# Kernel tuning notes

Hardware: AMD Instinct MI355X
Metric: run time of the kernel (lower is better)

Reference implementation:

```python
import jax, jax.numpy as jnp
import numpy as np

B, BUFF, STK, NCOMP, HIST = 128, 64, 48, 8, 96
VOCAB, WDIM, POSN, POSD = 100000, 300, 50, 50
DEP, CAD, HAD, FC, U = 40, 50, 50, 128, 256
NOUT = 2 + 2 * DEP


def setup_inputs() -> dict:
    key = jax.random.key(0)
    ks = jax.random.split(key, 40)
    d = {}
    d['buff_word_id'] = jax.random.randint(ks[0], (B, BUFF), 0, VOCAB)
    d['buff_pos_id'] = jax.random.randint(ks[1], (B, BUFF), 0, POSN)
    d['comp_word_id'] = jax.random.randint(ks[2], (B, STK, 2 * NCOMP), 0, VOCAB)
    d['comp_pos_id'] = jax.random.randint(ks[3], (B, STK, 2 * NCOMP), 0, POSN)
    d['comp_action_id'] = jax.random.randint(ks[4], (B, STK, NCOMP), 0, 2 * DEP)
    d['comp_action_len'] = jax.random.randint(ks[5], (B, STK), 0, NCOMP + 1)
    d['history_action_id'] = jax.random.randint(ks[6], (B, HIST), 0, 3 + 4 * DEP)
    d['stack_length'] = jax.random.randint(ks[7], (B,), 1, STK + 1)
    d['buff_length'] = jax.random.randint(ks[8], (B,), 1, BUFF + 1)
    d['history_action_length'] = jax.random.randint(ks[9], (B,), 1, HIST + 1)

    def w(k, shape):
        return jax.random.normal(k, shape, jnp.float32) / np.sqrt(shape[0])

    d['p_emb'] = jax.random.normal(ks[10], (POSN, POSD), jnp.float32) * 0.1
    d['comp_a_emb'] = jax.random.normal(ks[11], (2 * DEP, CAD), jnp.float32) * 0.1
    d['hist_a_emb'] = jax.random.normal(ks[12], (3 + 4 * DEP, HAD), jnp.float32) * 0.1
    d['w_emb'] = jax.random.normal(ks[13], (VOCAB, WDIM), jnp.float32) * 0.1
    d['emb_W'] = w(ks[14], (WDIM + POSD, FC)); d['emb_b'] = jnp.zeros((FC,), jnp.float32)
    d['rec_W'] = w(ks[15], (FC + CAD + FC, FC)); d['rec_b'] = jnp.zeros((FC,), jnp.float32)
    d['sW0'] = w(ks[16], (FC + U, 4 * U)); d['sb0'] = jnp.zeros((4 * U,), jnp.float32)
    d['sW1'] = w(ks[17], (U + U, 4 * U)); d['sb1'] = jnp.zeros((4 * U,), jnp.float32)
    d['bW0'] = w(ks[18], (FC + U, 4 * U)); d['bb0'] = jnp.zeros((4 * U,), jnp.float32)
    d['bW1'] = w(ks[19], (U + U, 4 * U)); d['bb1'] = jnp.zeros((4 * U,), jnp.float32)
    d['aW0'] = w(ks[20], (HAD + U, 4 * U)); d['ab0'] = jnp.zeros((4 * U,), jnp.float32)
    d['aW1'] = w(ks[21], (U + U, 4 * U)); d['ab1'] = jnp.zeros((4 * U,), jnp.float32)
    d['fW'] = w(ks[22], (3 * U, NOUT)); d['fb'] = jnp.zeros((NOUT,), jnp.float32)
    return d


def _lstm_cell(c, h, x, W, b):
    # TF LSTMCell gate order: i, j (candidate), f, o; forget_bias = 1.0
    z = jnp.concatenate([x, h], -1) @ W + b
    i, j, f, o = jnp.split(z, 4, -1)
    c = c * jax.nn.sigmoid(f + 1.0) + jax.nn.sigmoid(i) * jnp.tanh(j)
    h = jnp.tanh(c) * jax.nn.sigmoid(o)
    return c, h


def _run_lstm2(x, lengths, W0, b0, W1, b1):
    # x: [B, T, D]; returns final (at t = length) second-layer h, like dynamic_rnn's state[1].h
    Bb, T, _ = x.shape
    u = W0.shape[1] // 4
    init = tuple(jnp.zeros((Bb, u), x.dtype) for _ in range(4))

    def step(carry, inp):
        xt, t = inp
        c0, h0, c1, h1 = carry
        nc0, nh0 = _lstm_cell(c0, h0, xt, W0, b0)
        nc1, nh1 = _lstm_cell(c1, h1, nh0, W1, b1)
        m = (t < lengths)[:, None]
        new = tuple(jnp.where(m, n, o) for n, o in zip((nc0, nh0, nc1, nh1), carry))
        return new, None

    (c0, h0, c1, h1), _ = jax.lax.scan(step, init, (x.transpose(1, 0, 2), jnp.arange(T)))
    return h1


def _compose(word_id, comp_emb, act_emb, a_len, rec_W, rec_b):
    # word_id: [2N] int, comp_emb: [2N, FC], act_emb: [N, CAD], a_len: scalar
    # Sequential dict-keyed recursive composition (dict keys are head word ids).
    N = act_emb.shape[0]
    head_ids = word_id[0::2]
    dep_ids = word_id[1::2]
    idxs = jnp.arange(N)

    def step(vals, n):
        mask_h = (head_ids == head_ids[n]) & (idxs < n)
        mask_d = (head_ids == dep_ids[n]) & (idxs < n)
        ih = jnp.max(jnp.where(mask_h, idxs, -1))
        idd = jnp.max(jnp.where(mask_d, idxs, -1))
        head_e = jnp.where(ih >= 0, vals[jnp.maximum(ih, 0)], comp_emb[2 * n])
        dep_e = jnp.where(idd >= 0, vals[jnp.maximum(idd, 0)], comp_emb[2 * n + 1])
        new = jnp.tanh(jnp.concatenate([head_e, act_emb[n], dep_e]) @ rec_W + rec_b)
        return vals.at[n].set(new), new

    vals0 = jnp.zeros((N, rec_W.shape[1]), comp_emb.dtype)
    _, news = jax.lax.scan(step, vals0, idxs)
    return jnp.where(a_len == 0, comp_emb[0], news[jnp.maximum(a_len - 1, 0)])


def reference(buff_word_id, buff_pos_id, comp_word_id, comp_pos_id, comp_action_id,
              comp_action_len, history_action_id, stack_length, buff_length,
              history_action_length, p_emb, comp_a_emb, hist_a_emb, w_emb,
              emb_W, emb_b, rec_W, rec_b, sW0, sb0, sW1, sb1, bW0, bb0, bW1, bb1,
              aW0, ab0, aW1, ab1, fW, fb):
    buff_emb = jax.nn.relu(
        jnp.concatenate([w_emb[buff_word_id], p_emb[buff_pos_id]], -1) @ emb_W + emb_b)
    comp_emb = jax.nn.relu(
        jnp.concatenate([w_emb[comp_word_id], p_emb[comp_pos_id]], -1) @ emb_W + emb_b)
    act_emb = comp_a_emb[comp_action_id]        # [B, STK, N, CAD]
    hist_emb = hist_a_emb[history_action_id]    # [B, HIST, HAD]

    comp_fn = lambda wi, ce, ae, al: _compose(wi, ce, ae, al, rec_W, rec_b)
    stack_emb = jax.vmap(jax.vmap(comp_fn))(comp_word_id, comp_emb, act_emb, comp_action_len)

    h_s = _run_lstm2(stack_emb, stack_length, sW0, sb0, sW1, sb1)
    h_b = _run_lstm2(buff_emb, buff_length, bW0, bb0, bW1, bb1)
    h_a = _run_lstm2(hist_emb, history_action_length, aW0, ab0, aW1, ab1)
    return jnp.concatenate([h_s, h_b, h_a], -1) @ fW + fb
```

## Files before the change

kernel.cpp:

```cpp
#include <hip/hip_runtime.h>

#define BB    128
#define BUFF  64
#define STK   48
#define NCOMP 8
#define HIST  96
#define WDIM  300
#define POSD  50
#define CAD   50
#define HAD   50
#define FC    128
#define UU    256
#define NOUT  82

typedef __bf16 bf16;
typedef __attribute__((ext_vector_type(8))) __bf16 bf16x8;
typedef __attribute__((ext_vector_type(4))) float   f32x4;

__device__ __forceinline__ float sigf(float x)   { return 1.f / (1.f + __expf(-x)); }
__device__ __forceinline__ float tanhf_(float x) { return 1.f - 2.f / (1.f + __expf(2.f * x)); }

__device__ __forceinline__ unsigned pack2(const float* p) {
  union { unsigned u; bf16 h[2]; } r;
  r.h[0] = (bf16)p[0]; r.h[1] = (bf16)p[1];
  return r.u;
}

__global__ __launch_bounds__(256) void k_emb(
    const int* bw, const int* bp, const int* cw, const int* cp,
    const float* w_emb, const float* p_emb, const float* embW, const float* embB,
    bf16* comp_emb, bf16* buff_emb)
{
  __shared__ __align__(16) char sm[138752];
  bf16*  A  = (bf16*)sm;
  bf16*  Wt = (bf16*)(sm + 46080);
  float* sb = (float*)(sm + 46080 + 92160);

  const int tid = threadIdx.x;
  const int r0  = blockIdx.x * 64;

  for (int i = tid; i < 64 * 176; i += 256) {
    int m = i / 176, c2 = i % 176, e0 = 2 * c2;
    int r = r0 + m;
    unsigned v;
    if (e0 < 300) {
      int word = (r < 98304) ? cw[r] : bw[r - 98304];
      v = pack2(w_emb + word * 300 + e0);
    } else if (e0 < 350) {
      int pos = (r < 98304) ? cp[r] : bp[r - 98304];
      v = pack2(p_emb + pos * 50 + (e0 - 300));
    } else v = 0u;
    *(unsigned*)(A + m * 360 + e0) = v;
  }
  for (int i = tid; i < 350 * 128; i += 256) {
    int k = i >> 7, n = i & 127;
    Wt[n * 360 + k] = (bf16)embW[i];
  }
  { int i = tid; if (i < 256) { int n = i >> 1; Wt[n * 360 + 350 + (i & 1)] = (bf16)0.f; } }
  if (tid < 128) sb[tid] = embB[tid];
  __syncthreads();

  const int wv = tid >> 6, lane = tid & 63, l15 = lane & 15, quad = lane >> 4;
  f32x4 acc[8];
#pragma unroll
  for (int i = 0; i < 8; ++i) acc[i] = (f32x4){0.f, 0.f, 0.f, 0.f};

  const bf16* Arow = A + (wv * 16 + l15) * 360;
  for (int ks = 0; ks < 11; ++ks) {
    int kq = ks * 32 + quad * 8;
    bf16x8 a = *(const bf16x8*)(Arow + kq);
#pragma unroll
    for (int nt = 0; nt < 8; ++nt) {
      bf16x8 b = *(const bf16x8*)(Wt + (nt * 16 + l15) * 360 + kq);
      acc[nt] = __builtin_amdgcn_mfma_f32_16x16x32_bf16(a, b, acc[nt], 0, 0, 0);
    }
  }
#pragma unroll
  for (int nt = 0; nt < 8; ++nt)
#pragma unroll
    for (int rr = 0; rr < 4; ++rr) {
      int row = wv * 16 + quad * 4 + rr;
      int n   = nt * 16 + l15;
      float z = fmaxf(acc[nt][rr] + sb[n], 0.f);
      int r = r0 + row;
      bf16 o = (bf16)z;
      if (r < 98304) comp_emb[r * 128 + n] = o;
      else           buff_emb[(r - 98304) * 128 + n] = o;
    }
}

__global__ __launch_bounds__(256) void k_compose(
    const int* cw, const int* caid, const int* calen,
    const bf16* comp_emb, const float* ca_emb, const float* recW, const float* recB,
    bf16* stack_emb)
{
  __shared__ __align__(16) char sm[129344];
  bf16*  Wt   = (bf16*)sm;
  bf16*  X    = (bf16*)(sm + 83968);
  bf16*  VALS = (bf16*)(sm + 94464);
  float* recb = (float*)(sm + 127232);
  int*   IH   = (int*)(sm + 127744);
  int*   ID   = (int*)(sm + 128256);
  int*   AN   = (int*)(sm + 128768);
  int*   ALEN = (int*)(sm + 129280);

  const int tid = threadIdx.x;
  const int bs0 = blockIdx.x * 16;

  for (int i = tid; i < 306 * 128; i += 256) {
    int k = i >> 7, n = i & 127;
    Wt[n * 328 + k] = (bf16)recW[i];
  }
  for (int i = tid; i < 128 * 22; i += 256) {
    int n = i / 22, k = 306 + i % 22;
    Wt[n * 328 + k] = (bf16)0.f;
  }
  if (tid < 128) recb[tid] = recB[tid];
  if (tid < 16) {
    int bs = bs0 + tid;
    int hid[8], did[8];
#pragma unroll
    for (int m = 0; m < 8; ++m) { hid[m] = cw[bs * 16 + 2 * m]; did[m] = cw[bs * 16 + 2 * m + 1]; }
    for (int n = 0; n < 8; ++n) {
      int ih = -1, idd = -1;
      for (int m = 0; m < n; ++m) { if (hid[m] == hid[n]) ih = m; if (hid[m] == did[n]) idd = m; }
      IH[tid * 8 + n] = ih; ID[tid * 8 + n] = idd; AN[tid * 8 + n] = caid[bs * 8 + n];
    }
    ALEN[tid] = calen[bs];
  }
  __syncthreads();

  const int wv = tid >> 6, lane = tid & 63, l15 = lane & 15, quad = lane >> 4;

  for (int n = 0; n < 8; ++n) {
    for (int i = tid; i < 16 * 160; i += 256) {
      int p = i / 160, c2 = i % 160, e0 = 2 * c2;
      int bs = bs0 + p;
      unsigned v;
      if (e0 < 128) {
        int ih = IH[p * 8 + n];
        v = (ih >= 0) ? *(const unsigned*)(VALS + (p * 8 + ih) * 128 + e0)
                      : *(const unsigned*)(comp_emb + (bs * 16 + 2 * n) * 128 + e0);
      } else if (e0 < 178) {
        v = pack2(ca_emb + AN[p * 8 + n] * 50 + (e0 - 128));
      } else if (e0 < 306) {
        int e = e0 - 178;
        int idd = ID[p * 8 + n];
        v = (idd >= 0) ? *(const unsigned*)(VALS + (p * 8 + idd) * 128 + e)
                       : *(const unsigned*)(comp_emb + (bs * 16 + 2 * n + 1) * 128 + e);
      } else v = 0u;
      *(unsigned*)(X + p * 328 + e0) = v;
    }
    __syncthreads();

    f32x4 acc[2];
    acc[0] = (f32x4){0.f,0.f,0.f,0.f}; acc[1] = (f32x4){0.f,0.f,0.f,0.f};
    for (int ks = 0; ks < 10; ++ks) {
      int kq = ks * 32 + quad * 8;
      bf16x8 a = *(const bf16x8*)(X + l15 * 328 + kq);
#pragma unroll
      for (int t2 = 0; t2 < 2; ++t2) {
        int nt = 2 * wv + t2;
        bf16x8 b = *(const bf16x8*)(Wt + (nt * 16 + l15) * 328 + kq);
        acc[t2] = __builtin_amdgcn_mfma_f32_16x16x32_bf16(a, b, acc[t2], 0, 0, 0);
      }
    }
    __syncthreads();
#pragma unroll
    for (int t2 = 0; t2 < 2; ++t2) {
      int nt = 2 * wv + t2;
#pragma unroll
      for (int rr = 0; rr < 4; ++rr) {
        int p = quad * 4 + rr;
        int col = nt * 16 + l15;
        VALS[(p * 8 + n) * 128 + col] = (bf16)tanhf_(acc[t2][rr] + recb[col]);
      }
    }
    __syncthreads();
  }

  for (int i = tid; i < 16 * 64; i += 256) {
    int p = i / 64, c2 = i % 64, e0 = 2 * c2;
    int bs = bs0 + p;
    int al = ALEN[p];
    unsigned v = (al == 0) ? *(const unsigned*)(comp_emb + (bs * 16) * 128 + e0)
                           : *(const unsigned*)(VALS + (p * 8 + (al - 1)) * 128 + e0);
    *(unsigned*)(stack_emb + bs * 128 + e0) = v;
  }
}

struct BarT { int cnt; int pad[31]; };

template<bool COH>
__device__ __forceinline__ bf16x8 hload(const bf16* p) {
  bf16x8 v;
  if constexpr (COH)
    asm volatile("global_load_dwordx4 %0, %1, off sc0" : "=v"(v) : "v"(p) : "memory");
  else
    asm volatile("global_load_dwordx4 %0, %1, off sc0 sc1" : "=v"(v) : "v"(p) : "memory");
  return v;
}

template<bool COH>
__device__ __forceinline__ void hstore(bf16* p, unsigned long long v) {
  if constexpr (COH)
    asm volatile("global_store_dwordx2 %0, %1, off" :: "v"(p), "v"(v) : "memory");
  else
    __hip_atomic_store((unsigned long long*)p, v, __ATOMIC_RELAXED, __HIP_MEMORY_SCOPE_AGENT);
}

template<int L, int LAYER, bool COH>
__device__ __forceinline__ void lstm_role(
    const float* W, const float* bias,
    const bf16* xsrc, const float* hist_tab, const int* hist_id,
    const int* lenp, bf16* h0w, bf16* h1w, BarT* bar, char* sm, int u0)
{
  constexpr int T   = (L == 0) ? STK : (L == 1) ? BUFF : HIST;
  constexpr int K   = (LAYER == 0) ? ((L == 2) ? 320 : 384) : 512;
  constexpr int KP  = K + 8;
  constexpr int Kxp = (LAYER == 0) ? ((L == 2) ? 64 : 128) : 256;
  constexpr int Tx  = (L == 0) ? STK : BUFF;

  const int tid = threadIdx.x;
  bf16*  Wt     = (bf16*)sm;
  bf16*  hstage = (bf16*)(sm + 128 * KP * 2);
  float* sb     = (float*)(sm + 128 * KP * 2 + 9216);
  bf16*  Xa     = (bf16*)(sm + 128 * KP * 2 + 9216 + 512);

  for (int i = tid; i < K * 128; i += 256) {
    int kk = i >> 7, cc = i & 127;
    int col = (cc >> 5) * 256 + u0 + (cc & 31);
    bf16 v;
    if (LAYER == 0 && L == 2) {
      if (kk < 64) v = (kk < 50) ? (bf16)W[kk * 1024 + col] : (bf16)0.f;
      else         v = (bf16)W[(kk - 14) * 1024 + col];
    } else v = (bf16)W[kk * 1024 + col];
    Wt[cc * KP + kk] = v;
  }
  if (tid < 128) { int col = (tid >> 5) * 256 + u0 + (tid & 31); sb[tid] = bias[col]; }

  const int wv = tid >> 6, lane = tid & 63, l15 = lane & 15, quad = lane >> 4;
  int lenr[8];
#pragma unroll
  for (int mt = 0; mt < 2; ++mt)
#pragma unroll
    for (int rr = 0; rr < 4; ++rr)
      lenr[mt * 4 + rr] = lenp[32 * wv + 16 * mt + quad * 4 + rr];

  float cst[16], hst[16];
#pragma unroll
  for (int i = 0; i < 16; ++i) { cst[i] = 0.f; hst[i] = 0.f; }

  const int row0 = 32 * wv + l15;

  __syncthreads();

  for (int p = 0; p <= T; ++p) {
    const bool active = (LAYER == 0) ? (p < T) : (p >= 1);
    const int  t = (LAYER == 0) ? p : (p - 1);

    if (L == 2 && LAYER == 0 && active) {
      for (int i = tid; i < 128 * 32; i += 256) {
        int row = i >> 5, e0 = 2 * (i & 31);
        unsigned v = 0u;
        if (e0 < 50) { int id = hist_id[row * 96 + t]; v = pack2(hist_tab + id * 50 + e0); }
        *(unsigned*)(Xa + row * 72 + e0) = v;
      }
    }
    __syncthreads();

    if (active) {
      const bf16* h0r = h0w + ((p - 1) & 1) * 32768;
      const bf16* h1r = h1w + (p & 1) * 32768;

      bf16x8 hA[16];
#pragma unroll
      for (int hk = 0; hk < 8; ++hk)
#pragma unroll
        for (int mt = 0; mt < 2; ++mt)
          hA[hk * 2 + mt] = hload<COH>(h0r + (row0 + 16 * mt) * 256 + hk * 32 + quad * 8);
      bf16x8 hB[16];
      if (LAYER == 1) {
#pragma unroll
        for (int hk = 0; hk < 8; ++hk)
#pragma unroll
          for (int mt = 0; mt < 2; ++mt)
            hB[hk * 2 + mt] = hload<COH>(h1r + (row0 + 16 * mt) * 256 + hk * 32 + quad * 8);
      }

      f32x4 acc[2][8];
#pragma unroll
      for (int a1 = 0; a1 < 2; ++a1)
#pragma unroll
        for (int a2 = 0; a2 < 8; ++a2) acc[a1][a2] = (f32x4){0.f, 0.f, 0.f, 0.f};

      if (LAYER == 0) {
#pragma unroll
        for (int ks = 0; ks < Kxp / 32; ++ks) {
          int kq = ks * 32 + quad * 8;
          bf16x8 a[2];
#pragma unroll
          for (int mt = 0; mt < 2; ++mt) {
            int row = row0 + 16 * mt;
            if (L == 2) a[mt] = *(const bf16x8*)(Xa + row * 72 + kq);
            else        a[mt] = *(const bf16x8*)(xsrc + (row * Tx + t) * 128 + kq);
          }
#pragma unroll
          for (int nt = 0; nt < 8; ++nt) {
            bf16x8 b = *(const bf16x8*)(Wt + (nt * 16 + l15) * KP + kq);
            acc[0][nt] = __builtin_amdgcn_mfma_f32_16x16x32_bf16(a[0], b, acc[0][nt], 0, 0, 0);
            acc[1][nt] = __builtin_amdgcn_mfma_f32_16x16x32_bf16(a[1], b, acc[1][nt], 0, 0, 0);
          }
        }
      }

      asm volatile("s_waitcnt vmcnt(0)" ::: "memory");
      __builtin_amdgcn_sched_barrier(0);

      constexpr int HB0 = (LAYER == 0) ? Kxp : 0;
#pragma unroll
      for (int hk = 0; hk < 8; ++hk) {
        int kq = HB0 + hk * 32 + quad * 8;
#pragma unroll
        for (int nt = 0; nt < 8; ++nt) {
          bf16x8 b = *(const bf16x8*)(Wt + (nt * 16 + l15) * KP + kq);
          acc[0][nt] = __builtin_amdgcn_mfma_f32_16x16x32_bf16(hA[hk * 2 + 0], b, acc[0][nt], 0, 0, 0);
          acc[1][nt] = __builtin_amdgcn_mfma_f32_16x16x32_bf16(hA[hk * 2 + 1], b, acc[1][nt], 0, 0, 0);
        }
      }
      if (LAYER == 1) {
#pragma unroll
        for (int hk = 0; hk < 8; ++hk) {
          int kq = 256 + hk * 32 + quad * 8;
#pragma unroll
          for (int nt = 0; nt < 8; ++nt) {
            bf16x8 b = *(const bf16x8*)(Wt + (nt * 16 + l15) * KP + kq);
            acc[0][nt] = __builtin_amdgcn_mfma_f32_16x16x32_bf16(hB[hk * 2 + 0], b, acc[0][nt], 0, 0, 0);
            acc[1][nt] = __builtin_amdgcn_mfma_f32_16x16x32_bf16(hB[hk * 2 + 1], b, acc[1][nt], 0, 0, 0);
          }
        }
      }

#pragma unroll
      for (int mt = 0; mt < 2; ++mt)
#pragma unroll
        for (int g2 = 0; g2 < 2; ++g2)
#pragma unroll
          for (int rr = 0; rr < 4; ++rr) {
            int row = 32 * wv + 16 * mt + quad * 4 + rr;
            float zi = acc[mt][0 + g2][rr] + sb[(0 + g2) * 16 + l15];
            float zj = acc[mt][2 + g2][rr] + sb[(2 + g2) * 16 + l15];
            float zf = acc[mt][4 + g2][rr] + sb[(4 + g2) * 16 + l15];
            float zo = acc[mt][6 + g2][rr] + sb[(6 + g2) * 16 + l15];
            float ig = sigf(zi), jg = tanhf_(zj), fg = sigf(zf + 1.f), og = sigf(zo);
            int idx = mt * 8 + g2 * 4 + rr;
            float cn = cst[idx] * fg + ig * jg;
            float hn = tanhf_(cn) * og;
            bool mk = (t < lenr[mt * 4 + rr]);
            cst[idx] = mk ? cn : cst[idx];
            hst[idx] = mk ? hn : hst[idx];
            hstage[row * 36 + g2 * 16 + l15] = (bf16)hst[idx];
          }
    }
    __syncthreads();
    if (active) {
      bf16* dst = (LAYER == 0) ? (h0w + (p & 1) * 32768) : (h1w + ((p - 1) & 1) * 32768);
      for (int i = tid; i < 128 * 8; i += 256) {
        int row = i >> 3, c = i & 7;
        unsigned long long v = *(const unsigned long long*)(hstage + row * 36 + c * 4);
        hstore<COH>(dst + row * 256 + u0 + c * 4, v);
      }
    }
    if (p < T) {
      __syncthreads();
      if (tid == 0) {
        __builtin_amdgcn_sched_barrier(0);
        const int target = 16 * (p + 1);
        int prev = __hip_atomic_fetch_add(&bar->cnt, 1, __ATOMIC_RELAXED, __HIP_MEMORY_SCOPE_AGENT);
        if (prev != target - 1) {
          while (__hip_atomic_load(&bar->cnt, __ATOMIC_RELAXED, __HIP_MEMORY_SCOPE_AGENT) < target) { }
        }
        __builtin_amdgcn_sched_barrier(0);
      }
      __syncthreads();
    }
  }
}

__global__ __launch_bounds__(256, 1) void k_lstm(
    const float* sW0, const float* sb0, const float* sW1, const float* sb1,
    const float* bW0, const float* bb0, const float* bW1, const float* bb1,
    const float* aW0, const float* ab0, const float* aW1, const float* ab1,
    const bf16* stack_emb, const bf16* buff_emb, const float* hist_tab, const int* hist_id,
    const int* len_s, const int* len_b, const int* len_a,
    bf16* h0buf, bf16* h1buf, BarT* bars, BarT* cbars, int* taken, int* xcctab, int* probes)
{
  __shared__ __align__(16) char sm[143872];
  __shared__ int s_role[3];
  const int tid = threadIdx.x;

  if (tid == 0) {
    int xcc = __builtin_amdgcn_s_getreg(6164) & 0xF;
    int l = -1, r = -1;
    if (xcc < 3) {
      int st = blockIdx.x & 15;
      for (int ii = 0; ii < 16 && l < 0; ++ii) {
        int i = (st + ii) & 15;
        int exp0 = 0;
        if (__hip_atomic_compare_exchange_strong(&taken[xcc * 16 + i], &exp0, 1,
              __ATOMIC_RELAXED, __ATOMIC_RELAXED, __HIP_MEMORY_SCOPE_AGENT)) { l = xcc; r = i; }
      }
    }
    if (l < 0) {
      unsigned long long t0 = __builtin_amdgcn_s_memrealtime();
      while (__builtin_amdgcn_s_memrealtime() - t0 < 10000ULL) __builtin_amdgcn_s_sleep(16);
      for (int i = 0; i < 48 && l < 0; ++i) {
        int exp0 = 0;
        if (__hip_atomic_compare_exchange_strong(&taken[i], &exp0, 1,
              __ATOMIC_RELAXED, __ATOMIC_RELAXED, __HIP_MEMORY_SCOPE_AGENT)) { l = i >> 4; r = i & 15; }
      }
    }
    s_role[0] = l; s_role[1] = r; s_role[2] = 0;
    if (l >= 0) {
      __hip_atomic_store(&xcctab[l * 16 + r], xcc + 1, __ATOMIC_RELAXED, __HIP_MEMORY_SCOPE_AGENT);
      int* pp = &probes[l * 16 + r];
      int tok = r + 1;
      asm volatile("global_store_dword %0, %1, off" :: "v"(pp), "v"(tok) : "memory");
      asm volatile("s_waitcnt vmcnt(0)" ::: "memory");
      __hip_atomic_fetch_add(&cbars[l].cnt, 1, __ATOMIC_RELAXED, __HIP_MEMORY_SCOPE_AGENT);
      while (__hip_atomic_load(&cbars[l].cnt, __ATOMIC_RELAXED, __HIP_MEMORY_SCOPE_AGENT) < 16)
        __builtin_amdgcn_s_sleep(1);
      int myx = xcc + 1, coh = 1;
      for (int i = 0; i < 16; ++i)
        coh &= (__hip_atomic_load(&xcctab[l * 16 + i], __ATOMIC_RELAXED, __HIP_MEMORY_SCOPE_AGENT) == myx);
      for (int i = 0; i < 16; ++i) {
        int* qp = &probes[l * 16 + i];
        int pv;
        asm volatile("global_load_dword %0, %1, off sc0" : "=v"(pv) : "v"(qp) : "memory");
        asm volatile("s_waitcnt vmcnt(0)" ::: "memory");
        coh &= (pv == i + 1);
      }
      s_role[2] = coh;
    }
  }
  __syncthreads();

  const int l = s_role[0];
  if (l < 0) return;
  const int rid = s_role[1], coh = s_role[2];
  const int layer = rid >> 3;
  const int u0    = (rid & 7) * 32;

  BarT* bar = bars + l;
  bf16* h0w = h0buf + l * 2 * 32768;
  bf16* h1w = h1buf + l * 2 * 32768;

  const float *W0_, *b0_, *W1_, *b1_; const bf16* xs_; const int* lenp_;
  if (l == 0)      { W0_ = sW0; b0_ = sb0; W1_ = sW1; b1_ = sb1; xs_ = stack_emb; lenp_ = len_s; }
  else if (l == 1) { W0_ = bW0; b0_ = bb0; W1_ = bW1; b1_ = bb1; xs_ = buff_emb;  lenp_ = len_b; }
  else             { W0_ = aW0; b0_ = ab0; W1_ = aW1; b1_ = ab1; xs_ = nullptr;   lenp_ = len_a; }
  const float* W  = layer ? W1_ : W0_;
  const float* bi = layer ? b1_ : b0_;

  switch (l * 4 + layer * 2 + coh) {
    case  0: lstm_role<0, 0, false>(W, bi, xs_, hist_tab, hist_id, lenp_, h0w, h1w, bar, sm, u0); break;
    case  1: lstm_role<0, 0, true >(W, bi, xs_, hist_tab, hist_id, lenp_, h0w, h1w, bar, sm, u0); break;
    case  2: lstm_role<0, 1, false>(W, bi, xs_, hist_tab, hist_id, lenp_, h0w, h1w, bar, sm, u0); break;
    case  3: lstm_role<0, 1, true >(W, bi, xs_, hist_tab, hist_id, lenp_, h0w, h1w, bar, sm, u0); break;
    case  4: lstm_role<1, 0, false>(W, bi, xs_, hist_tab, hist_id, lenp_, h0w, h1w, bar, sm, u0); break;
    case  5: lstm_role<1, 0, true >(W, bi, xs_, hist_tab, hist_id, lenp_, h0w, h1w, bar, sm, u0); break;
    case  6: lstm_role<1, 1, false>(W, bi, xs_, hist_tab, hist_id, lenp_, h0w, h1w, bar, sm, u0); break;
    case  7: lstm_role<1, 1, true >(W, bi, xs_, hist_tab, hist_id, lenp_, h0w, h1w, bar, sm, u0); break;
    case  8: lstm_role<2, 0, false>(W, bi, xs_, hist_tab, hist_id, lenp_, h0w, h1w, bar, sm, u0); break;
    case  9: lstm_role<2, 0, true >(W, bi, xs_, hist_tab, hist_id, lenp_, h0w, h1w, bar, sm, u0); break;
    case 10: lstm_role<2, 1, false>(W, bi, xs_, hist_tab, hist_id, lenp_, h0w, h1w, bar, sm, u0); break;
    case 11: lstm_role<2, 1, true >(W, bi, xs_, hist_tab, hist_id, lenp_, h0w, h1w, bar, sm, u0); break;
  }
}

__global__ __launch_bounds__(128) void k_final(
    const bf16* h1buf, const float* fW, const float* fb, float* out)
{
  __shared__ float hs[768];
  const int b = blockIdx.x, tid = threadIdx.x;
  for (int i = tid; i < 768; i += 128) {
    int L = i >> 8, u = i & 255;
    hs[i] = (float)h1buf[(L * 2 + 1) * 32768 + b * 256 + u];
  }
  __syncthreads();
  if (tid < NOUT) {
    float acc = fb[tid];
    for (int u = 0; u < 768; ++u) acc += hs[u] * fW[u * NOUT + tid];
    out[b * NOUT + tid] = acc;
  }
}

extern "C" void kernel_launch(void* const* d_in, const int* in_sizes, int n_in,
                              void* d_out, int out_size, void* d_ws, size_t ws_size,
                              hipStream_t stream)
{
  (void)in_sizes; (void)n_in; (void)out_size; (void)ws_size;
  char* ws = (char*)d_ws;
  BarT* bars   = (BarT*)ws;
  BarT* cbars  = (BarT*)(ws + 512);
  int*  taken  = (int*)(ws + 1024);
  int*  xcctab = (int*)(ws + 1280);
  int*  probes = (int*)(ws + 1536);
  bf16* h0buf  = (bf16*)(ws + 2048);
  bf16* h1buf  = (bf16*)(ws + 2048 + 393216);
  bf16* comp_emb  = (bf16*)(ws + 788480);
  bf16* buff_emb  = (bf16*)(ws + 788480 + 25165824);
  bf16* stack_emb = (bf16*)(ws + 788480 + 25165824 + 2097152);

  hipMemsetAsync(ws, 0, 788480, stream);

  k_emb<<<1664, 256, 0, stream>>>(
      (const int*)d_in[0], (const int*)d_in[1], (const int*)d_in[2], (const int*)d_in[3],
      (const float*)d_in[13], (const float*)d_in[10], (const float*)d_in[14], (const float*)d_in[15],
      comp_emb, buff_emb);

  k_compose<<<384, 256, 0, stream>>>(
      (const int*)d_in[2], (const int*)d_in[4], (const int*)d_in[5],
      comp_emb, (const float*)d_in[11], (const float*)d_in[16], (const float*)d_in[17],
      stack_emb);

  k_lstm<<<256, 256, 0, stream>>>(
      (const float*)d_in[18], (const float*)d_in[19], (const float*)d_in[20], (const float*)d_in[21],
      (const float*)d_in[22], (const float*)d_in[23], (const float*)d_in[24], (const float*)d_in[25],
      (const float*)d_in[26], (const float*)d_in[27], (const float*)d_in[28], (const float*)d_in[29],
      stack_emb, buff_emb, (const float*)d_in[12], (const int*)d_in[6],
      (const int*)d_in[7], (const int*)d_in[8], (const int*)d_in[9],
      h0buf, h1buf, bars, cbars, taken, xcctab, probes);

  k_final<<<128, 128, 0, stream>>>(h1buf, (const float*)d_in[30], (const float*)d_in[31],
                                   (float*)d_out);
}
```

Before: 1.888 ms.

## Split LSTM recurrent block across 8 waves with 16 rows each

Doubles the LSTM kernel's block size from 256 to 512 threads, so each of 8 wavefronts owns one 16-row M tile instead of two. Per-wave MFMA chains, hidden-state register arrays and gate math are halved, aiming to shorten the serial per-timestep critical path in the persistent recurrent loop. The cost is more waves per CU contending for LDS weight reads, plus syncthreads over a larger block. Weight load, staging and store loops are restrided to match.

Result: faster. 1.702 ms (-9.9%).

```diff
diff --git a/kernel.cpp b/kernel.cpp
--- a/kernel.cpp
+++ b/kernel.cpp
@@ -227,7 +227,7 @@
   float* sb     = (float*)(sm + 128 * KP * 2 + 9216);
   bf16*  Xa     = (bf16*)(sm + 128 * KP * 2 + 9216 + 512);
 
-  for (int i = tid; i < K * 128; i += 256) {
+  for (int i = tid; i < K * 128; i += 512) {
     int kk = i >> 7, cc = i & 127;
     int col = (cc >> 5) * 256 + u0 + (cc & 31);
     bf16 v;
@@ -240,18 +240,15 @@
   if (tid < 128) { int col = (tid >> 5) * 256 + u0 + (tid & 31); sb[tid] = bias[col]; }
 
   const int wv = tid >> 6, lane = tid & 63, l15 = lane & 15, quad = lane >> 4;
-  int lenr[8];
-#pragma unroll
-  for (int mt = 0; mt < 2; ++mt)
-#pragma unroll
-    for (int rr = 0; rr < 4; ++rr)
-      lenr[mt * 4 + rr] = lenp[32 * wv + 16 * mt + quad * 4 + rr];
-
-  float cst[16], hst[16];
-#pragma unroll
-  for (int i = 0; i < 16; ++i) { cst[i] = 0.f; hst[i] = 0.f; }
-
-  const int row0 = 32 * wv + l15;
+  const int row0 = 16 * wv + l15;
+  int lenr[4];
+#pragma unroll
+  for (int rr = 0; rr < 4; ++rr)
+    lenr[rr] = lenp[16 * wv + quad * 4 + rr];
+
+  float cst[8], hst[8];
+#pragma unroll
+  for (int i = 0; i < 8; ++i) { cst[i] = 0.f; hst[i] = 0.f; }
 
   __syncthreads();
 
@@ -260,7 +257,7 @@
     const int  t = (LAYER == 0) ? p : (p - 1);
 
     if (L == 2 && LAYER == 0 && active) {
-      for (int i = tid; i < 128 * 32; i += 256) {
+      for (int i = tid; i < 128 * 32; i += 512) {
         int row = i >> 5, e0 = 2 * (i & 31);
         unsigned v = 0u;
         if (e0 < 50) { int id = hist_id[row * 96 + t]; v = pack2(hist_tab + id * 50 + e0); }
@@ -273,43 +270,32 @@
       const bf16* h0r = h0w + ((p - 1) & 1) * 32768;
       const bf16* h1r = h1w + (p & 1) * 32768;
 
-      bf16x8 hA[16];
+      bf16x8 hA[8];
 #pragma unroll
       for (int hk = 0; hk < 8; ++hk)
-#pragma unroll
-        for (int mt = 0; mt < 2; ++mt)
-          hA[hk * 2 + mt] = hload<COH>(h0r + (row0 + 16 * mt) * 256 + hk * 32 + quad * 8);
-      bf16x8 hB[16];
+        hA[hk] = hload<COH>(h0r + row0 * 256 + hk * 32 + quad * 8);
+      bf16x8 hB[8];
       if (LAYER == 1) {
 #pragma unroll
         for (int hk = 0; hk < 8; ++hk)
-#pragma unroll
-          for (int mt = 0; mt < 2; ++mt)
-            hB[hk * 2 + mt] = hload<COH>(h1r + (row0 + 16 * mt) * 256 + hk * 32 + quad * 8);
-      }
-
-      f32x4 acc[2][8];
-#pragma unroll
-      for (int a1 = 0; a1 < 2; ++a1)
-#pragma unroll
-        for (int a2 = 0; a2 < 8; ++a2) acc[a1][a2] = (f32x4){0.f, 0.f, 0.f, 0.f};
+          hB[hk] = hload<COH>(h1r + row0 * 256 + hk * 32 + quad * 8);
+      }
+
+      f32x4 acc[8];
+#pragma unroll
+      for (int a2 = 0; a2 < 8; ++a2) acc[a2] = (f32x4){0.f, 0.f, 0.f, 0.f};
 
       if (LAYER == 0) {
 #pragma unroll
         for (int ks = 0; ks < Kxp / 32; ++ks) {
           int kq = ks * 32 + quad * 8;
-          bf16x8 a[2];
-#pragma unroll
-          for (int mt = 0; mt < 2; ++mt) {
-            int row = row0 + 16 * mt;
-            if (L == 2) a[mt] = *(const bf16x8*)(Xa + row * 72 + kq);
-            else        a[mt] = *(const bf16x8*)(xsrc + (row * Tx + t) * 128 + kq);
-          }
+          bf16x8 a;
+          if (L == 2) a = *(const bf16x8*)(Xa + row0 * 72 + kq);
+          else        a = *(const bf16x8*)(xsrc + (row0 * Tx + t) * 128 + kq);
 #pragma unroll
           for (int nt = 0; nt < 8; ++nt) {
             bf16x8 b = *(const bf16x8*)(Wt + (nt * 16 + l15) * KP + kq);
-            acc[0][nt] = __builtin_amdgcn_mfma_f32_16x16x32_bf16(a[0], b, acc[0][nt], 0, 0, 0);
-            acc[1][nt] = __builtin_amdgcn_mfma_f32_16x16x32_bf16(a[1], b, acc[1][nt], 0, 0, 0);
+            acc[nt] = __builtin_amdgcn_mfma_f32_16x16x32_bf16(a, b, acc[nt], 0, 0, 0);
           }
         }
       }
@@ -324,8 +310,7 @@
 #pragma unroll
         for (int nt = 0; nt < 8; ++nt) {
           bf16x8 b = *(const bf16x8*)(Wt + (nt * 16 + l15) * KP + kq);
-          acc[0][nt] = __builtin_amdgcn_mfma_f32_16x16x32_bf16(hA[hk * 2 + 0], b, acc[0][nt], 0, 0, 0);
-          acc[1][nt] = __builtin_amdgcn_mfma_f32_16x16x32_bf16(hA[hk * 2 + 1], b, acc[1][nt], 0, 0, 0);
+          acc[nt] = __builtin_amdgcn_mfma_f32_16x16x32_bf16(hA[hk], b, acc[nt], 0, 0, 0);
         }
       }
       if (LAYER == 1) {
@@ -335,37 +320,34 @@
 #pragma unroll
           for (int nt = 0; nt < 8; ++nt) {
             bf16x8 b = *(const bf16x8*)(Wt + (nt * 16 + l15) * KP + kq);
-            acc[0][nt] = __builtin_amdgcn_mfma_f32_16x16x32_bf16(hB[hk * 2 + 0], b, acc[0][nt], 0, 0, 0);
-            acc[1][nt] = __builtin_amdgcn_mfma_f32_16x16x32_bf16(hB[hk * 2 + 1], b, acc[1][nt], 0, 0, 0);
+            acc[nt] = __builtin_amdgcn_mfma_f32_16x16x32_bf16(hB[hk], b, acc[nt], 0, 0, 0);
           }
         }
       }
 
 #pragma unroll
-      for (int mt = 0; mt < 2; ++mt)
-#pragma unroll
-        for (int g2 = 0; g2 < 2; ++g2)
-#pragma unroll
-          for (int rr = 0; rr < 4; ++rr) {
-            int row = 32 * wv + 16 * mt + quad * 4 + rr;
-            float zi = acc[mt][0 + g2][rr] + sb[(0 + g2) * 16 + l15];
-            float zj = acc[mt][2 + g2][rr] + sb[(2 + g2) * 16 + l15];
-            float zf = acc[mt][4 + g2][rr] + sb[(4 + g2) * 16 + l15];
-            float zo = acc[mt][6 + g2][rr] + sb[(6 + g2) * 16 + l15];
-            float ig = sigf(zi), jg = tanhf_(zj), fg = sigf(zf + 1.f), og = sigf(zo);
-            int idx = mt * 8 + g2 * 4 + rr;
-            float cn = cst[idx] * fg + ig * jg;
-            float hn = tanhf_(cn) * og;
-            bool mk = (t < lenr[mt * 4 + rr]);
-            cst[idx] = mk ? cn : cst[idx];
-            hst[idx] = mk ? hn : hst[idx];
-            hstage[row * 36 + g2 * 16 + l15] = (bf16)hst[idx];
-          }
+      for (int g2 = 0; g2 < 2; ++g2)
+#pragma unroll
+        for (int rr = 0; rr < 4; ++rr) {
+          int row = 16 * wv + quad * 4 + rr;
+          float zi = acc[0 + g2][rr] + sb[(0 + g2) * 16 + l15];
+          float zj = acc[2 + g2][rr] + sb[(2 + g2) * 16 + l15];
+          float zf = acc[4 + g2][rr] + sb[(4 + g2) * 16 + l15];
+          float zo = acc[6 + g2][rr] + sb[(6 + g2) * 16 + l15];
+          float ig = sigf(zi), jg = tanhf_(zj), fg = sigf(zf + 1.f), og = sigf(zo);
+          int idx = g2 * 4 + rr;
+          float cn = cst[idx] * fg + ig * jg;
+          float hn = tanhf_(cn) * og;
+          bool mk = (t < lenr[rr]);
+          cst[idx] = mk ? cn : cst[idx];
+          hst[idx] = mk ? hn : hst[idx];
+          hstage[row * 36 + g2 * 16 + l15] = (bf16)hst[idx];
+        }
     }
     __syncthreads();
     if (active) {
       bf16* dst = (LAYER == 0) ? (h0w + (p & 1) * 32768) : (h1w + ((p - 1) & 1) * 32768);
-      for (int i = tid; i < 128 * 8; i += 256) {
+      for (int i = tid; i < 128 * 8; i += 512) {
         int row = i >> 3, c = i & 7;
         unsigned long long v = *(const unsigned long long*)(hstage + row * 36 + c * 4);
         hstore<COH>(dst + row * 256 + u0 + c * 4, v);
@@ -387,7 +369,7 @@
   }
 }
 
-__global__ __launch_bounds__(256, 1) void k_lstm(
+__global__ __launch_bounds__(512, 1) void k_lstm(
     const float* sW0, const float* sb0, const float* sW1, const float* sb1,
     const float* bW0, const float* bb0, const float* bW1, const float* bb1,
     const float* aW0, const float* ab0, const float* aW1, const float* ab1,
@@ -524,7 +506,7 @@
       comp_emb, (const float*)d_in[11], (const float*)d_in[16], (const float*)d_in[17],
       stack_emb);
 
-  k_lstm<<<256, 256, 0, stream>>>(
+  k_lstm<<<256, 512, 0, stream>>>(
       (const float*)d_in[18], (const float*)d_in[19], (const float*)d_in[20], (const float*)d_in[21],
       (const float*)d_in[22], (const float*)d_in[23], (const float*)d_in[24], (const float*)d_in[25],
       (const float*)d_in[26], (const float*)d_in[27], (const float*)d_in[28], (const float*)d_in[29],
```
